# Kernel tuning notes

Measured on AMD Instinct MI355X. Metric: run time of the kernel, lower is better.

## Reference

```python
import jax, jax.numpy as jnp
import numpy as np

EMBED = 1024
D_FF = 4 * EMBED
N_EXPERTS = 8
TOP_K = 2
B, S = 2, 1024


def setup_inputs() -> dict:
    key = jax.random.key(0)
    ks = jax.random.split(key, 10)
    sc_d = 1.0 / np.sqrt(EMBED)
    sc_h = 1.0 / np.sqrt(D_FF)
    return {
        "inputs": jax.random.normal(ks[0], (B, S, EMBED), jnp.float32),
        # router MLP: Linear(D,4D) -> ReLU -> Linear(4D,E)
        "rw1": jax.random.normal(ks[1], (EMBED, D_FF), jnp.float32) * sc_d,
        "rb1": jnp.zeros((D_FF,), jnp.float32),
        "rw2": jax.random.normal(ks[2], (D_FF, N_EXPERTS), jnp.float32) * sc_h,
        "rb2": jnp.zeros((N_EXPERTS,), jnp.float32),
        # stacked expert weights: Linear(D,4D) -> ReLU -> Linear(4D,D)
        "W1": jax.random.normal(ks[3], (N_EXPERTS, EMBED, D_FF), jnp.float32) * sc_d,
        "b1": jnp.zeros((N_EXPERTS, D_FF), jnp.float32),
        "W2": jax.random.normal(ks[4], (N_EXPERTS, D_FF, EMBED), jnp.float32) * sc_h,
        "b2": jnp.zeros((N_EXPERTS, EMBED), jnp.float32),
    }


def reference(inputs, rw1, rb1, rw2, rb2, W1, b1, W2, b2):
    Bb, Ss, D = inputs.shape
    T = Bb * Ss
    xf = inputs.reshape(T, D)  # [T, D]

    # Router: scores over experts, keep top-k, softmax over kept entries only.
    score = jax.nn.relu(xf @ rw1 + rb1) @ rw2 + rb2          # [T, E]
    _, topi = jax.lax.top_k(score, TOP_K)                    # [T, K]
    mask = jnp.zeros(score.shape, bool).at[jnp.arange(T)[:, None], topi].set(True)
    gate = jax.nn.softmax(jnp.where(mask, score, -jnp.inf), axis=-1)  # [T, E]

    # Dense per-expert MLP weighted by gate; gate==0 for non-top-k experts,
    # matching the original masked gather/scatter exactly.
    out = jnp.zeros_like(xf)
    for e in range(N_EXPERTS):
        h = jax.nn.relu(xf @ W1[e] + b1[e])                  # [T, 4D]
        y = h @ W2[e] + b2[e]                                # [T, D]
        out = out + gate[:, e:e + 1] * y
    return out.reshape(Bb, Ss, D)
```

## Files before the change

### kernel.cpp

```cpp
#include <hip/hip_runtime.h>
#include <stdint.h>

typedef unsigned short ushort_t;
typedef __attribute__((ext_vector_type(8))) short short8;
typedef __attribute__((ext_vector_type(4))) float f32x4;

#define EMBED   1024
#define DFF     4096
#define NEXP    8
#define TOKENS  2048
#define SLOTS   4096
#define TMAX    40
#define TG      ((TMAX + 7) / 8)

__device__ __forceinline__ ushort_t f2bf(float f) {
  unsigned u = __float_as_uint(f);
  u += 0x7FFFu + ((u >> 16) & 1u);
  return (ushort_t)(u >> 16);
}
__device__ __forceinline__ float bf2f(ushort_t b) {
  return __uint_as_float(((unsigned)b) << 16);
}

__device__ __forceinline__ void gl2lds16(const void* g, void* l) {
  typedef const __attribute__((address_space(1))) unsigned char* gp_t;
  typedef __attribute__((address_space(3))) unsigned char* lp_t;
  __builtin_amdgcn_global_load_lds((gp_t)(uintptr_t)g, (lp_t)(uintptr_t)l, 16, 0, 0);
}

__device__ __forceinline__ void transp_body(const float* __restrict__ src,
                                            ushort_t* __restrict__ dst,
                                            int src_ld, int dst_ld, int bx, int by,
                                            int dst_koff, int lo, float (*t)[65])
{
  int n0 = bx * 64, k0 = by * 64;
  int tid = threadIdx.x;
  int kk = tid >> 4, nn = (tid & 15) * 4;
  #pragma unroll
  for (int it = 0; it < 4; it++) {
    float4 v = *(const float4*)(src + (size_t)(k0 + kk + it * 16) * src_ld + n0 + nn);
    t[kk + it * 16][nn]     = v.x;
    t[kk + it * 16][nn + 1] = v.y;
    t[kk + it * 16][nn + 2] = v.z;
    t[kk + it * 16][nn + 3] = v.w;
  }
  __syncthreads();
  int nn2 = tid >> 3, kk2 = (tid & 7) * 8;
  #pragma unroll
  for (int it = 0; it < 2; it++) {
    int n = nn2 + it * 32;
    union { ushort_t u[8]; uint4 v; } pk;
    #pragma unroll
    for (int j = 0; j < 8; j++) {
      float xv = t[kk2 + j][n];
      ushort_t hv = f2bf(xv);
      pk.u[j] = lo ? f2bf(xv - bf2f(hv)) : hv;
    }
    *(uint4*)(dst + (size_t)(n0 + n) * dst_ld + dst_koff + k0 + kk2) = pk.v;
  }
}

__global__ void transp_conv(const float* __restrict__ src, ushort_t* __restrict__ dst,
                            int src_ld, int dst_ld, long src_estride, long dst_estride,
                            int dst_koff, int lo)
{
  __shared__ __align__(16) float t[64][65];
  transp_body(src + (size_t)blockIdx.z * src_estride,
              dst + (size_t)blockIdx.z * dst_estride,
              src_ld, dst_ld, blockIdx.x, blockIdx.y, dst_koff, lo, t);
}

__global__ __launch_bounds__(256) void prep_kernel(const float* __restrict__ x,
    ushort_t* __restrict__ Xs, const float* __restrict__ rw1,
    ushort_t* __restrict__ RW1t, int* __restrict__ counts)
{
  __shared__ __align__(16) float tt[64][65];
  int bid = blockIdx.x;
  if (bid < TOKENS) {
    if (bid == 0 && threadIdx.x < NEXP) counts[threadIdx.x] = 0;
    int d = threadIdx.x * 4;
    float4 v = *(const float4*)(x + (size_t)bid * EMBED + d);
    ushort4 hi, lo;
    hi.x = f2bf(v.x); lo.x = f2bf(v.x - bf2f(hi.x));
    hi.y = f2bf(v.y); lo.y = f2bf(v.y - bf2f(hi.y));
    hi.z = f2bf(v.z); lo.z = f2bf(v.z - bf2f(hi.z));
    hi.w = f2bf(v.w); lo.w = f2bf(v.w - bf2f(hi.w));
    ushort_t* row = Xs + (size_t)bid * 2048;
    *(ushort4*)(row + d)        = hi;
    *(ushort4*)(row + 1024 + d) = lo;
    return;
  }
  int idx = bid - TOKENS;
  int which = idx >> 10, sub = idx & 1023;
  transp_body(rw1, RW1t, DFF, 3072, sub & 63, sub >> 6, which * 1024, which == 2, tt);
}

template<int APATH, int OUTMODE, bool RELU, bool EXPERT, int SPLITK, int NX, int NFUSE>
__global__ __launch_bounds__(256, 3)
void gemm_kernel(const ushort_t* __restrict__ A, const ushort_t* __restrict__ B,
                 const float* __restrict__ bias, void* __restrict__ Cout,
                 const float* __restrict__ slot_gate, const int* __restrict__ slot_token,
                 const int* __restrict__ off, const int* __restrict__ tile_e,
                 const int* __restrict__ tile_y, int e0, int e1,
                 int M, int N, int K, int ngb,
                 const float* __restrict__ tsrc0, ushort_t* __restrict__ tdst0,
                 const float* __restrict__ tsrc1, ushort_t* __restrict__ tdst1)
{
  __shared__ __align__(16) char lds_raw[49152];
  auto As = (ushort_t(*)[4096])lds_raw;
  auto Bs = (ushort_t(*)[4096])(lds_raw + 24576);

  if constexpr (NFUSE > 0) {
    int bidf = blockIdx.x;
    if (bidf >= ngb) {
      int idx = bidf - ngb;
      auto tt = (float(*)[65])lds_raw;
      const size_t ES = (size_t)EMBED * DFF;
      if (idx < 64 * 16 * 8) {
        int bx = idx & 63, by = (idx >> 6) & 15, z = idx >> 10;
        transp_body(tsrc0 + z * ES, tdst0 + z * ES, DFF, EMBED, bx, by, 0, 0, tt);
      } else {
        idx -= 64 * 16 * 8;
        int bx = idx & 15, by = (idx >> 4) & 63, z = idx >> 10;
        transp_body(tsrc1 + z * ES, tdst1 + z * ES, EMBED, DFF, bx, by, 0, 0, tt);
      }
      return;
    }
  }

  int e = 0, kc = 0, row0, col0, m_base, m_cnt;
  if (EXPERT) {
    constexpr int INNER = NX * SPLITK;
    int bid = blockIdx.x;
    int xcd = bid & 7;
    int j   = bid >> 3;
    int t   = xcd + 8 * (j / INNER);
    int i   = j % INNER;
    int xi  = i % NX;
    kc      = i / NX;
    e = tile_e[t];
    if (e < e0 || e >= e1) return;
    row0   = tile_y[t] * 128;
    col0   = xi * 128;
    m_base = off[e];
    m_cnt  = off[e + 1] - m_base;
  } else {
    int bid = blockIdx.x;
    row0 = (bid >> 5) * 128;
    col0 = (bid & 31) * 128;
    m_base = 0; m_cnt = M;
    if (row0 >= m_cnt) return;
  }
  const int Kc   = K / SPLITK;
  const int kbeg = kc * Kc;

  const int tid  = threadIdx.x;
  const int lane = tid & 63;
  const int wid  = tid >> 6;
  const int wm = wid & 1, wn = wid >> 1;

  const int srow  = lane >> 2;
  const int schk8 = ((lane & 3) ^ ((lane >> 3) & 3)) * 8;

  const ushort_t* gA[2];
  const ushort_t* gB[2];
  int aoff[2];
  const ushort_t* Bt = B + (EXPERT ? (size_t)(e - e0) * (size_t)N * K : 0);
  #pragma unroll
  for (int h = 0; h < 2; h++) {
    int r  = row0 + h * 64 + wid * 16 + srow;
    int rl = min(r, m_cnt - 1);
    size_t rowb;
    if (APATH == 2)      rowb = (size_t)slot_token[m_base + rl] * 2048;
    else if (APATH == 1) rowb = (size_t)rl * 2048;
    else                 rowb = (size_t)(m_base + rl) * (size_t)K;
    gA[h]   = A + rowb + (APATH == 0 ? kbeg : 0) + schk8;
    aoff[h] = (h * 64 + wid * 16) * 32;

    int n = col0 + h * 64 + wid * 16 + srow;
    gB[h] = Bt + (size_t)n * K + kbeg + schk8;
  }

  auto stage = [&](int pb, int kt) {
    const int k0 = kt << 5;
    const int k0a = (APATH == 1 && k0 >= 2048) ? k0 - 2048 : k0;
    #pragma unroll
    for (int h = 0; h < 2; h++) {
      gl2lds16(gA[h] + k0a, &As[pb][aoff[h]]);
      gl2lds16(gB[h] + k0,  &Bs[pb][aoff[h]]);
    }
  };

  f32x4 acc[4][4];
  #pragma unroll
  for (int i = 0; i < 4; i++)
    #pragma unroll
    for (int j = 0; j < 4; j++)
      acc[i][j] = (f32x4){0.f, 0.f, 0.f, 0.f};

  const int q  = lane >> 4;
  const int rr = lane & 15;
  const int sw8 = (q ^ ((rr >> 1) & 3)) * 8;
  const int abase = (wm * 64 + rr) * 32 + sw8;
  const int bbase = (wn * 64 + rr) * 32 + sw8;

  const int nkt = Kc >> 5;

  stage(0, 0);
  if (nkt > 1) stage(1, 1);

  for (int kt = 0; kt < nkt; kt++) {
    if (kt + 1 < nkt) asm volatile("s_waitcnt vmcnt(4)" ::: "memory");
    else              asm volatile("s_waitcnt vmcnt(0)" ::: "memory");
    __builtin_amdgcn_s_barrier();
    __builtin_amdgcn_sched_barrier(0);
    if (kt + 2 < nkt) stage((kt + 2) % 3, kt + 2);

    const int cur = kt % 3;
    short8 af[4], bfr[4];
    #pragma unroll
    for (int i = 0; i < 4; i++) {
      af[i]  = *(const short8*)(&As[cur][abase + i * 512]);
      bfr[i] = *(const short8*)(&Bs[cur][bbase + i * 512]);
    }
    asm volatile("s_waitcnt lgkmcnt(0)" ::: "memory");
    __builtin_amdgcn_sched_barrier(0);
    #pragma unroll
    for (int mt = 0; mt < 4; mt++)
      #pragma unroll
      for (int nt = 0; nt < 4; nt++)
        acc[mt][nt] = __builtin_amdgcn_mfma_f32_16x16x32_bf16(af[mt], bfr[nt], acc[mt][nt], 0, 0, 0);
  }

  const float* biasp = bias + (EXPERT ? (size_t)e * N : 0);
  float bv[4];
  #pragma unroll
  for (int nt = 0; nt < 4; nt++)
    bv[nt] = biasp[col0 + wn * 64 + nt * 16 + rr];
  const float bscale = (SPLITK == 1 || kc == 0) ? 1.f : 0.f;

  if constexpr (OUTMODE == 4) {
    const float* rw2p = slot_gate;
    float4 wa[4], wb[4];
    #pragma unroll
    for (int nt = 0; nt < 4; nt++) {
      int c = col0 + wn * 64 + nt * 16 + rr;
      wa[nt] = *(const float4*)(rw2p + (size_t)c * 8);
      wb[nt] = *(const float4*)(rw2p + (size_t)c * 8 + 4);
    }
    float* Ps = (float*)Cout;
    const int xi2 = (col0 >> 6) + wn;
    #pragma unroll
    for (int mt = 0; mt < 4; mt++) {
      #pragma unroll
      for (int i = 0; i < 4; i++) {
        float4 sA = {0.f, 0.f, 0.f, 0.f}, sB = {0.f, 0.f, 0.f, 0.f};
        #pragma unroll
        for (int nt = 0; nt < 4; nt++) {
          float v = acc[mt][nt][i] + bv[nt];
          if (RELU) v = fmaxf(v, 0.f);
          sA.x += v * wa[nt].x; sA.y += v * wa[nt].y;
          sA.z += v * wa[nt].z; sA.w += v * wa[nt].w;
          sB.x += v * wb[nt].x; sB.y += v * wb[nt].y;
          sB.z += v * wb[nt].z; sB.w += v * wb[nt].w;
        }
        #pragma unroll
        for (int o = 1; o <= 8; o <<= 1) {
          sA.x += __shfl_xor(sA.x, o); sA.y += __shfl_xor(sA.y, o);
          sA.z += __shfl_xor(sA.z, o); sA.w += __shfl_xor(sA.w, o);
          sB.x += __shfl_xor(sB.x, o); sB.y += __shfl_xor(sB.y, o);
          sB.z += __shfl_xor(sB.z, o); sB.w += __shfl_xor(sB.w, o);
        }
        if (rr == 0) {
          int row = row0 + wm * 64 + mt * 16 + q * 4 + i;
          float* p = Ps + ((size_t)row * 64 + xi2) * 8;
          *(float4*)p       = sA;
          *(float4*)(p + 4) = sB;
        }
      }
    }
  } else {
    #pragma unroll
    for (int mt = 0; mt < 4; mt++) {
      #pragma unroll
      for (int i = 0; i < 4; i++) {
        int r_loc = row0 + wm * 64 + mt * 16 + q * 4 + i;
        if (r_loc < m_cnt) {
          int slot = m_base + r_loc;
          float g = 1.f;
          if (OUTMODE == 3) g = slot_gate[slot];
          #pragma unroll
          for (int nt = 0; nt < 4; nt++) {
            float v = acc[mt][nt][i] + bscale * bv[nt];
            if (RELU) v = fmaxf(v, 0.f);
            int c = col0 + wn * 64 + nt * 16 + rr;
            if (OUTMODE == 0)      ((float*)Cout)[(size_t)slot * N + c]    = v;
            else if (OUTMODE == 1) ((ushort_t*)Cout)[(size_t)slot * N + c] = f2bf(v);
            else ((float*)Cout)[((size_t)kc * SLOTS + slot) * N + c] = g * v;
          }
        }
      }
    }
  }
}

__global__ void router_reduce(const float* __restrict__ Ps, const float* __restrict__ rb2,
                              int* __restrict__ topi, float* __restrict__ gates,
                              int* __restrict__ counts)
{
  int t = blockIdx.x * 4 + (threadIdx.x >> 6);
  if (t >= TOKENS) return;
  int lane = threadIdx.x & 63;
  const float* pt = Ps + (size_t)t * 512;
  float4 v0 = *(const float4*)(pt + lane * 8);
  float4 v1 = *(const float4*)(pt + lane * 8 + 4);
  #pragma unroll
  for (int o = 1; o <= 32; o <<= 1) {
    v0.x += __shfl_xor(v0.x, o); v0.y += __shfl_xor(v0.y, o);
    v0.z += __shfl_xor(v0.z, o); v0.w += __shfl_xor(v0.w, o);
    v1.x += __shfl_xor(v1.x, o); v1.y += __shfl_xor(v1.y, o);
    v1.z += __shfl_xor(v1.z, o); v1.w += __shfl_xor(v1.w, o);
  }
  if (lane == 0) {
    float s[8] = {v0.x + rb2[0], v0.y + rb2[1], v0.z + rb2[2], v0.w + rb2[3],
                  v1.x + rb2[4], v1.y + rb2[5], v1.z + rb2[6], v1.w + rb2[7]};
    int i0 = 0;
    #pragma unroll
    for (int e = 1; e < 8; e++) if (s[e] > s[i0]) i0 = e;
    int i1 = (i0 == 0) ? 1 : 0;
    #pragma unroll
    for (int e = 0; e < 8; e++) if (e != i0 && s[e] > s[i1]) i1 = e;
    float ex = __expf(s[i1] - s[i0]);
    float g0 = 1.f / (1.f + ex);
    float g1 = ex / (1.f + ex);
    topi[t * 2] = i0; topi[t * 2 + 1] = i1;
    gates[t * 2] = g0; gates[t * 2 + 1] = g1;
    atomicAdd(&counts[i0], 1);
    atomicAdd(&counts[i1], 1);
  }
}

__global__ void assign_all(const int* __restrict__ counts, const int* __restrict__ topi,
                           const float* __restrict__ gates, int* __restrict__ off,
                           int* __restrict__ tile_e, int* __restrict__ tile_y,
                           int* __restrict__ slot_token, float* __restrict__ slot_gate,
                           int* __restrict__ tok_slot)
{
  __shared__ int s_off[NEXP];
  __shared__ int s_cur[NEXP];
  int tid = threadIdx.x;
  if (tid < NEXP) s_cur[tid] = 0;
  if (tid == 0) {
    int a = 0, t = 0;
    for (int e = 0; e < NEXP; e++) {
      off[e] = a; s_off[e] = a;
      int c = counts[e]; a += c;
      int ty = (c + 127) >> 7;
      for (int y = 0; y < ty; y++) { tile_e[t] = e; tile_y[t] = y; t++; }
    }
    off[NEXP] = a;
    for (; t < TMAX; t++) { tile_e[t] = -1; tile_y[t] = 0; }
  }
  __syncthreads();
  for (int t = tid; t < TOKENS; t += 256) {
    #pragma unroll
    for (int k = 0; k < 2; k++) {
      int e = topi[t * 2 + k];
      int p = atomicAdd(&s_cur[e], 1);
      int s = s_off[e] + p;
      slot_token[s] = t;
      slot_gate[s]  = gates[t * 2 + k];
      tok_slot[t * 2 + k] = s;
    }
  }
}

template<int NC>
__global__ void combine_out(const float* __restrict__ Ys, const int* __restrict__ tok_slot,
                            float* __restrict__ out)
{
  int t = blockIdx.x;
  int d = threadIdx.x * 4;
  int s0 = tok_slot[t * 2], s1 = tok_slot[t * 2 + 1];
  float4 o = {0.f, 0.f, 0.f, 0.f};
  #pragma unroll
  for (int k = 0; k < NC; k++) {
    float4 a = *(const float4*)(Ys + ((size_t)k * SLOTS + s0) * EMBED + d);
    float4 b = *(const float4*)(Ys + ((size_t)k * SLOTS + s1) * EMBED + d);
    o.x += a.x + b.x;
    o.y += a.y + b.y;
    o.z += a.z + b.z;
    o.w += a.w + b.w;
  }
  *(float4*)(out + (size_t)t * EMBED + d) = o;
}

extern "C" void kernel_launch(void* const* d_in, const int* in_sizes, int n_in,
                              void* d_out, int out_size, void* d_ws, size_t ws_size,
                              hipStream_t stream)
{
  const float* x   = (const float*)d_in[0];
  const float* rw1 = (const float*)d_in[1];
  const float* rb1 = (const float*)d_in[2];
  const float* rw2 = (const float*)d_in[3];
  const float* rb2 = (const float*)d_in[4];
  const float* W1  = (const float*)d_in[5];
  const float* b1  = (const float*)d_in[6];
  const float* W2  = (const float*)d_in[7];
  const float* b2  = (const float*)d_in[8];
  float* out = (float*)d_out;
  char* ws = (char*)d_ws;

  const long W1ES = (long)EMBED * DFF;
  const long W2ES = (long)DFF * EMBED;
  const size_t SZ_R = (size_t)4096 * 4096 * 2;

  const bool FULL = ws_size >= ((size_t)300 << 20);

  if (FULL) {
    char* p = ws;
    ushort_t* W1T  = (ushort_t*)p;  p += (size_t)NEXP * DFF * EMBED * 2;
    ushort_t* W2T  = (ushort_t*)p;  p += (size_t)NEXP * EMBED * DFF * 2;
    ushort_t* RW1t = (ushort_t*)p;  p += (size_t)4096 * 3072 * 2;
    ushort_t* Hs   = (ushort_t*)p;  p += (size_t)SLOTS * DFF * 2;
    ushort_t* Xhl  = (ushort_t*)p;  p += (size_t)TOKENS * 2048 * 2;
    float*    Ys   = (float*)p;     p += (size_t)4 * SLOTS * EMBED * 4;
    float*    Ps   = (float*)p;     p += (size_t)TOKENS * 512 * 4;
    int*   topi       = (int*)p;    p += TOKENS * 2 * 4;
    float* gates      = (float*)p;  p += TOKENS * 2 * 4;
    int*   tok_slot   = (int*)p;    p += TOKENS * 2 * 4;
    int*   slot_token = (int*)p;    p += SLOTS * 4;
    float* slot_gate  = (float*)p;  p += SLOTS * 4;
    int*   counts     = (int*)p;    p += 256;
    int*   off        = (int*)p;    p += 256;
    int*   tile_e     = (int*)p;    p += 256;
    int*   tile_y     = (int*)p;    p += 256;

    prep_kernel<<<TOKENS + 3 * 1024, 256, 0, stream>>>(x, Xhl, rw1, RW1t, counts);

    gemm_kernel<1, 4, true, false, 1, 32, 2>
        <<<dim3(512 + 16384, 1, 1), 256, 0, stream>>>(Xhl, RW1t, rb1, Ps, rw2,
            nullptr, nullptr, nullptr, nullptr, 0, NEXP, TOKENS, DFF, 3072,
            512, W1, W1T, W2, W2T);

    router_reduce<<<512, 256, 0, stream>>>(Ps, rb2, topi, gates, counts);
    assign_all<<<1, 256, 0, stream>>>(counts, topi, gates, off, tile_e, tile_y,
                                      slot_token, slot_gate, tok_slot);

    gemm_kernel<2, 1, true, true, 1, 32, 0>
        <<<dim3(8 * TG * 32, 1, 1), 256, 0, stream>>>(Xhl, W1T, b1, Hs,
            nullptr, slot_token, off, tile_e, tile_y, 0, NEXP, 0, DFF, EMBED,
            0, nullptr, nullptr, nullptr, nullptr);

    gemm_kernel<0, 3, false, true, 4, 8, 0>
        <<<dim3(8 * TG * 32, 1, 1), 256, 0, stream>>>(Hs, W2T, b2, Ys,
            slot_gate, nullptr, off, tile_e, tile_y, 0, NEXP, 0, EMBED, DFF,
            0, nullptr, nullptr, nullptr, nullptr);

    combine_out<4><<<TOKENS, 256, 0, stream>>>(Ys, tok_slot, out);
  } else {
    ushort_t* RW1t = (ushort_t*)ws;
    ushort_t* WT   = (ushort_t*)ws;
    ushort_t* Hs   = (ushort_t*)(ws + SZ_R);
    ushort_t* Xhl  = (ushort_t*)(ws + 2 * SZ_R);
    float*    Ys   = (float*)(ws + 2 * SZ_R);
    char* p = ws + 3 * SZ_R;
    float* Ps         = (float*)p;  p += (size_t)TOKENS * 512 * 4;
    int*   topi       = (int*)p;    p += TOKENS * 2 * 4;
    float* gates      = (float*)p;  p += TOKENS * 2 * 4;
    int*   tok_slot   = (int*)p;    p += TOKENS * 2 * 4;
    int*   slot_token = (int*)p;    p += SLOTS * 4;
    float* slot_gate  = (float*)p;  p += SLOTS * 4;
    int*   counts     = (int*)p;    p += 256;
    int*   off        = (int*)p;    p += 256;
    int*   tile_e     = (int*)p;    p += 256;
    int*   tile_y     = (int*)p;    p += 256;

    prep_kernel<<<TOKENS + 3 * 1024, 256, 0, stream>>>(x, Xhl, rw1, RW1t, counts);

    gemm_kernel<1, 4, true, false, 1, 32, 0>
        <<<dim3(512, 1, 1), 256, 0, stream>>>(Xhl, RW1t, rb1, Ps, rw2, nullptr,
            nullptr, nullptr, nullptr, 0, NEXP, TOKENS, DFF, 3072,
            0, nullptr, nullptr, nullptr, nullptr);
    router_reduce<<<512, 256, 0, stream>>>(Ps, rb2, topi, gates, counts);
    assign_all<<<1, 256, 0, stream>>>(counts, topi, gates, off, tile_e, tile_y,
                                      slot_token, slot_gate, tok_slot);

    for (int half = 0; half < 2; half++) {
      int e0 = half * 4;
      transp_conv<<<dim3(64, 16, 4), 256, 0, stream>>>(W1 + (size_t)e0 * W1ES, WT,
          DFF, EMBED, W1ES, W1ES, 0, 0);
      gemm_kernel<2, 1, true, true, 1, 32, 0>
          <<<dim3(8 * TG * 32, 1, 1), 256, 0, stream>>>(Xhl, WT, b1, Hs,
              nullptr, slot_token, off, tile_e, tile_y, e0, e0 + 4, 0, DFF, EMBED,
              0, nullptr, nullptr, nullptr, nullptr);
    }
    for (int half = 0; half < 2; half++) {
      int e0 = half * 4;
      transp_conv<<<dim3(16, 64, 4), 256, 0, stream>>>(W2 + (size_t)e0 * W2ES, WT,
          EMBED, DFF, W2ES, W2ES, 0, 0);
      gemm_kernel<0, 3, false, true, 2, 8, 0>
          <<<dim3(8 * TG * 16, 1, 1), 256, 0, stream>>>(Hs, WT, b2, Ys,
              slot_gate, nullptr, off, tile_e, tile_y, e0, e0 + 4, 0, EMBED, DFF,
              0, nullptr, nullptr, nullptr, nullptr);
    }

    combine_out<2><<<TOKENS, 256, 0, stream>>>(Ys, tok_slot, out);
  }
}
```

Baseline: 564.1 us.

## Shrink router GEMM tile to 64 rows and move W2 transpose into expert GEMM

```diff
diff --git a/kernel.cpp b/kernel.cpp
--- a/kernel.cpp
+++ b/kernel.cpp
@@ -95,34 +95,36 @@
   transp_body(rw1, RW1t, DFF, 3072, sub & 63, sub >> 6, which * 1024, which == 2, tt);
 }
 
-template<int APATH, int OUTMODE, bool RELU, bool EXPERT, int SPLITK, int NX, int NFUSE>
-__global__ __launch_bounds__(256, 3)
+template<int MT, int APATH, int OUTMODE, bool RELU, bool EXPERT, int SPLITK, int NX, int TSHAPE>
+__global__ __launch_bounds__(256, (MT == 64 ? 4 : 3))
 void gemm_kernel(const ushort_t* __restrict__ A, const ushort_t* __restrict__ B,
                  const float* __restrict__ bias, void* __restrict__ Cout,
                  const float* __restrict__ slot_gate, const int* __restrict__ slot_token,
                  const int* __restrict__ off, const int* __restrict__ tile_e,
                  const int* __restrict__ tile_y, int e0, int e1,
                  int M, int N, int K, int ngb,
-                 const float* __restrict__ tsrc0, ushort_t* __restrict__ tdst0,
-                 const float* __restrict__ tsrc1, ushort_t* __restrict__ tdst1)
-{
-  __shared__ __align__(16) char lds_raw[49152];
-  auto As = (ushort_t(*)[4096])lds_raw;
-  auto Bs = (ushort_t(*)[4096])(lds_raw + 24576);
-
-  if constexpr (NFUSE > 0) {
+                 const float* __restrict__ tsrc, ushort_t* __restrict__ tdst)
+{
+  constexpr int MH   = MT / 64;
+  constexpr int MACC = MT / 32;
+  constexpr int ASZ  = MT * 32;
+  constexpr int BSZ  = 128 * 32;
+  __shared__ __align__(16) char lds_raw[3 * (ASZ + BSZ) * 2];
+  auto As = (ushort_t(*)[ASZ])lds_raw;
+  auto Bs = (ushort_t(*)[BSZ])(lds_raw + 3 * ASZ * 2);
+
+  if constexpr (TSHAPE > 0) {
     int bidf = blockIdx.x;
     if (bidf >= ngb) {
       int idx = bidf - ngb;
       auto tt = (float(*)[65])lds_raw;
       const size_t ES = (size_t)EMBED * DFF;
-      if (idx < 64 * 16 * 8) {
+      if constexpr (TSHAPE == 1) {
         int bx = idx & 63, by = (idx >> 6) & 15, z = idx >> 10;
-        transp_body(tsrc0 + z * ES, tdst0 + z * ES, DFF, EMBED, bx, by, 0, 0, tt);
+        transp_body(tsrc + z * ES, tdst + z * ES, DFF, EMBED, bx, by, 0, 0, tt);
       } else {
-        idx -= 64 * 16 * 8;
         int bx = idx & 15, by = (idx >> 4) & 63, z = idx >> 10;
-        transp_body(tsrc1 + z * ES, tdst1 + z * ES, EMBED, DFF, bx, by, 0, 0, tt);
+        transp_body(tsrc + z * ES, tdst + z * ES, EMBED, DFF, bx, by, 0, 0, tt);
       }
       return;
     }
@@ -146,7 +148,7 @@
     m_cnt  = off[e + 1] - m_base;
   } else {
     int bid = blockIdx.x;
-    row0 = (bid >> 5) * 128;
+    row0 = (bid >> 5) * MT;
     col0 = (bid & 31) * 128;
     m_base = 0; m_cnt = M;
     if (row0 >= m_cnt) return;
@@ -164,10 +166,10 @@
 
   const ushort_t* gA[2];
   const ushort_t* gB[2];
-  int aoff[2];
+  int aoff[2], boff[2];
   const ushort_t* Bt = B + (EXPERT ? (size_t)(e - e0) * (size_t)N * K : 0);
   #pragma unroll
-  for (int h = 0; h < 2; h++) {
+  for (int h = 0; h < MH; h++) {
     int r  = row0 + h * 64 + wid * 16 + srow;
     int rl = min(r, m_cnt - 1);
     size_t rowb;
@@ -176,24 +178,26 @@
     else                 rowb = (size_t)(m_base + rl) * (size_t)K;
     gA[h]   = A + rowb + (APATH == 0 ? kbeg : 0) + schk8;
     aoff[h] = (h * 64 + wid * 16) * 32;
-
+  }
+  #pragma unroll
+  for (int h = 0; h < 2; h++) {
     int n = col0 + h * 64 + wid * 16 + srow;
-    gB[h] = Bt + (size_t)n * K + kbeg + schk8;
+    gB[h]   = Bt + (size_t)n * K + kbeg + schk8;
+    boff[h] = (h * 64 + wid * 16) * 32;
   }
 
   auto stage = [&](int pb, int kt) {
     const int k0 = kt << 5;
     const int k0a = (APATH == 1 && k0 >= 2048) ? k0 - 2048 : k0;
     #pragma unroll
-    for (int h = 0; h < 2; h++) {
-      gl2lds16(gA[h] + k0a, &As[pb][aoff[h]]);
-      gl2lds16(gB[h] + k0,  &Bs[pb][aoff[h]]);
-    }
+    for (int h = 0; h < MH; h++) gl2lds16(gA[h] + k0a, &As[pb][aoff[h]]);
+    #pragma unroll
+    for (int h = 0; h < 2; h++)  gl2lds16(gB[h] + k0,  &Bs[pb][boff[h]]);
   };
 
-  f32x4 acc[4][4];
-  #pragma unroll
-  for (int i = 0; i < 4; i++)
+  f32x4 acc[MACC][4];
+  #pragma unroll
+  for (int i = 0; i < MACC; i++)
     #pragma unroll
     for (int j = 0; j < 4; j++)
       acc[i][j] = (f32x4){0.f, 0.f, 0.f, 0.f};
@@ -201,7 +205,7 @@
   const int q  = lane >> 4;
   const int rr = lane & 15;
   const int sw8 = (q ^ ((rr >> 1) & 3)) * 8;
-  const int abase = (wm * 64 + rr) * 32 + sw8;
+  const int abase = (wm * (MT / 2) + rr) * 32 + sw8;
   const int bbase = (wn * 64 + rr) * 32 + sw8;
 
   const int nkt = Kc >> 5;
@@ -210,23 +214,28 @@
   if (nkt > 1) stage(1, 1);
 
   for (int kt = 0; kt < nkt; kt++) {
-    if (kt + 1 < nkt) asm volatile("s_waitcnt vmcnt(4)" ::: "memory");
-    else              asm volatile("s_waitcnt vmcnt(0)" ::: "memory");
+    if (kt + 1 < nkt) {
+      if constexpr (MT == 128) asm volatile("s_waitcnt vmcnt(4)" ::: "memory");
+      else                     asm volatile("s_waitcnt vmcnt(3)" ::: "memory");
+    } else {
+      asm volatile("s_waitcnt vmcnt(0)" ::: "memory");
+    }
     __builtin_amdgcn_s_barrier();
     __builtin_amdgcn_sched_barrier(0);
     if (kt + 2 < nkt) stage((kt + 2) % 3, kt + 2);
 
     const int cur = kt % 3;
-    short8 af[4], bfr[4];
-    #pragma unroll
-    for (int i = 0; i < 4; i++) {
+    short8 af[MACC], bfr[4];
+    #pragma unroll
+    for (int i = 0; i < MACC; i++)
       af[i]  = *(const short8*)(&As[cur][abase + i * 512]);
+    #pragma unroll
+    for (int i = 0; i < 4; i++)
       bfr[i] = *(const short8*)(&Bs[cur][bbase + i * 512]);
-    }
     asm volatile("s_waitcnt lgkmcnt(0)" ::: "memory");
     __builtin_amdgcn_sched_barrier(0);
     #pragma unroll
-    for (int mt = 0; mt < 4; mt++)
+    for (int mt = 0; mt < MACC; mt++)
       #pragma unroll
       for (int nt = 0; nt < 4; nt++)
         acc[mt][nt] = __builtin_amdgcn_mfma_f32_16x16x32_bf16(af[mt], bfr[nt], acc[mt][nt], 0, 0, 0);
@@ -251,7 +260,7 @@
     float* Ps = (float*)Cout;
     const int xi2 = (col0 >> 6) + wn;
     #pragma unroll
-    for (int mt = 0; mt < 4; mt++) {
+    for (int mt = 0; mt < MACC; mt++) {
       #pragma unroll
       for (int i = 0; i < 4; i++) {
         float4 sA = {0.f, 0.f, 0.f, 0.f}, sB = {0.f, 0.f, 0.f, 0.f};
@@ -272,7 +281,7 @@
           sB.z += __shfl_xor(sB.z, o); sB.w += __shfl_xor(sB.w, o);
         }
         if (rr == 0) {
-          int row = row0 + wm * 64 + mt * 16 + q * 4 + i;
+          int row = row0 + wm * (MT / 2) + mt * 16 + q * 4 + i;
           float* p = Ps + ((size_t)row * 64 + xi2) * 8;
           *(float4*)p       = sA;
           *(float4*)(p + 4) = sB;
@@ -281,10 +290,10 @@
     }
   } else {
     #pragma unroll
-    for (int mt = 0; mt < 4; mt++) {
+    for (int mt = 0; mt < MACC; mt++) {
       #pragma unroll
       for (int i = 0; i < 4; i++) {
-        int r_loc = row0 + wm * 64 + mt * 16 + q * 4 + i;
+        int r_loc = row0 + wm * (MT / 2) + mt * 16 + q * 4 + i;
         if (r_loc < m_cnt) {
           int slot = m_base + r_loc;
           float g = 1.f;
@@ -438,24 +447,24 @@
 
     prep_kernel<<<TOKENS + 3 * 1024, 256, 0, stream>>>(x, Xhl, rw1, RW1t, counts);
 
-    gemm_kernel<1, 4, true, false, 1, 32, 2>
-        <<<dim3(512 + 16384, 1, 1), 256, 0, stream>>>(Xhl, RW1t, rb1, Ps, rw2,
+    gemm_kernel<64, 1, 4, true, false, 1, 32, 1>
+        <<<dim3(1024 + 8192, 1, 1), 256, 0, stream>>>(Xhl, RW1t, rb1, Ps, rw2,
             nullptr, nullptr, nullptr, nullptr, 0, NEXP, TOKENS, DFF, 3072,
-            512, W1, W1T, W2, W2T);
+            1024, W1, W1T);
 
     router_reduce<<<512, 256, 0, stream>>>(Ps, rb2, topi, gates, counts);
     assign_all<<<1, 256, 0, stream>>>(counts, topi, gates, off, tile_e, tile_y,
                                       slot_token, slot_gate, tok_slot);
 
-    gemm_kernel<2, 1, true, true, 1, 32, 0>
-        <<<dim3(8 * TG * 32, 1, 1), 256, 0, stream>>>(Xhl, W1T, b1, Hs,
+    gemm_kernel<128, 2, 1, true, true, 1, 32, 2>
+        <<<dim3(8 * TG * 32 + 8192, 1, 1), 256, 0, stream>>>(Xhl, W1T, b1, Hs,
             nullptr, slot_token, off, tile_e, tile_y, 0, NEXP, 0, DFF, EMBED,
-            0, nullptr, nullptr, nullptr, nullptr);
-
-    gemm_kernel<0, 3, false, true, 4, 8, 0>
+            8 * TG * 32, W2, W2T);
+
+    gemm_kernel<128, 0, 3, false, true, 4, 8, 0>
         <<<dim3(8 * TG * 32, 1, 1), 256, 0, stream>>>(Hs, W2T, b2, Ys,
             slot_gate, nullptr, off, tile_e, tile_y, 0, NEXP, 0, EMBED, DFF,
-            0, nullptr, nullptr, nullptr, nullptr);
+            0, nullptr, nullptr);
 
     combine_out<4><<<TOKENS, 256, 0, stream>>>(Ys, tok_slot, out);
   } else {
@@ -478,10 +487,10 @@
 
     prep_kernel<<<TOKENS + 3 * 1024, 256, 0, stream>>>(x, Xhl, rw1, RW1t, counts);
 
-    gemm_kernel<1, 4, true, false, 1, 32, 0>
-        <<<dim3(512, 1, 1), 256, 0, stream>>>(Xhl, RW1t, rb1, Ps, rw2, nullptr,
+    gemm_kernel<64, 1, 4, true, false, 1, 32, 0>
+        <<<dim3(1024, 1, 1), 256, 0, stream>>>(Xhl, RW1t, rb1, Ps, rw2, nullptr,
             nullptr, nullptr, nullptr, 0, NEXP, TOKENS, DFF, 3072,
-            0, nullptr, nullptr, nullptr, nullptr);
+            0, nullptr, nullptr);
     router_reduce<<<512, 256, 0, stream>>>(Ps, rb2, topi, gates, counts);
     assign_all<<<1, 256, 0, stream>>>(counts, topi, gates, off, tile_e, tile_y,
                                       slot_token, slot_gate, tok_slot);
@@ -490,19 +499,19 @@
       int e0 = half * 4;
       transp_conv<<<dim3(64, 16, 4), 256, 0, stream>>>(W1 + (size_t)e0 * W1ES, WT,
           DFF, EMBED, W1ES, W1ES, 0, 0);
-      gemm_kernel<2, 1, true, true, 1, 32, 0>
+      gemm_kernel<128, 2, 1, true, true, 1, 32, 0>
           <<<dim3(8 * TG * 32, 1, 1), 256, 0, stream>>>(Xhl, WT, b1, Hs,
               nullptr, slot_token, off, tile_e, tile_y, e0, e0 + 4, 0, DFF, EMBED,
-              0, nullptr, nullptr, nullptr, nullptr);
+              0, nullptr, nullptr);
     }
     for (int half = 0; half < 2; half++) {
       int e0 = half * 4;
       transp_conv<<<dim3(16, 64, 4), 256, 0, stream>>>(W2 + (size_t)e0 * W2ES, WT,
           EMBED, DFF, W2ES, W2ES, 0, 0);
-      gemm_kernel<0, 3, false, true, 2, 8, 0>
+      gemm_kernel<128, 0, 3, false, true, 2, 8, 0>
           <<<dim3(8 * TG * 16, 1, 1), 256, 0, stream>>>(Hs, WT, b2, Ys,
               slot_gate, nullptr, off, tile_e, tile_y, e0, e0 + 4, 0, EMBED, DFF,
-              0, nullptr, nullptr, nullptr, nullptr);
+              0, nullptr, nullptr);
     }
 
     combine_out<2><<<TOKENS, 256, 0, stream>>>(Ys, tok_slot, out);
```

Result: slower. 583.1 us (+3.4%).

## Redistribute weight transposes across GEMM launches and shrink router transpose work

Applied to the files above, without the earlier changes.

```diff
diff --git a/kernel.cpp b/kernel.cpp
--- a/kernel.cpp
+++ b/kernel.cpp
@@ -91,11 +91,38 @@
     return;
   }
   int idx = bid - TOKENS;
-  int which = idx >> 10, sub = idx & 1023;
-  transp_body(rw1, RW1t, DFF, 3072, sub & 63, sub >> 6, which * 1024, which == 2, tt);
-}
-
-template<int APATH, int OUTMODE, bool RELU, bool EXPERT, int SPLITK, int NX, int NFUSE>
+  int n0 = (idx & 63) * 64, k0 = (idx >> 6) * 64;
+  int tid = threadIdx.x;
+  int kk = tid >> 4, nn = (tid & 15) * 4;
+  #pragma unroll
+  for (int it = 0; it < 4; it++) {
+    float4 v = *(const float4*)(rw1 + (size_t)(k0 + kk + it * 16) * DFF + n0 + nn);
+    tt[kk + it * 16][nn]     = v.x;
+    tt[kk + it * 16][nn + 1] = v.y;
+    tt[kk + it * 16][nn + 2] = v.z;
+    tt[kk + it * 16][nn + 3] = v.w;
+  }
+  __syncthreads();
+  int nn2 = tid >> 3, kk2 = (tid & 7) * 8;
+  #pragma unroll
+  for (int it = 0; it < 2; it++) {
+    int n = nn2 + it * 32;
+    union { ushort_t u[8]; uint4 v; } ph, pl;
+    #pragma unroll
+    for (int j = 0; j < 8; j++) {
+      float xv = tt[kk2 + j][n];
+      ushort_t hv = f2bf(xv);
+      ph.u[j] = hv;
+      pl.u[j] = f2bf(xv - bf2f(hv));
+    }
+    ushort_t* row = RW1t + (size_t)(n0 + n) * 3072 + k0 + kk2;
+    *(uint4*)(row)        = ph.v;
+    *(uint4*)(row + 1024) = ph.v;
+    *(uint4*)(row + 2048) = pl.v;
+  }
+}
+
+template<int APATH, int OUTMODE, bool RELU, bool EXPERT, int SPLITK, int NX, int TSHAPE>
 __global__ __launch_bounds__(256, 3)
 void gemm_kernel(const ushort_t* __restrict__ A, const ushort_t* __restrict__ B,
                  const float* __restrict__ bias, void* __restrict__ Cout,
@@ -103,26 +130,24 @@
                  const int* __restrict__ off, const int* __restrict__ tile_e,
                  const int* __restrict__ tile_y, int e0, int e1,
                  int M, int N, int K, int ngb,
-                 const float* __restrict__ tsrc0, ushort_t* __restrict__ tdst0,
-                 const float* __restrict__ tsrc1, ushort_t* __restrict__ tdst1)
+                 const float* __restrict__ tsrc, ushort_t* __restrict__ tdst)
 {
   __shared__ __align__(16) char lds_raw[49152];
   auto As = (ushort_t(*)[4096])lds_raw;
   auto Bs = (ushort_t(*)[4096])(lds_raw + 24576);
 
-  if constexpr (NFUSE > 0) {
+  if constexpr (TSHAPE > 0) {
     int bidf = blockIdx.x;
     if (bidf >= ngb) {
       int idx = bidf - ngb;
       auto tt = (float(*)[65])lds_raw;
       const size_t ES = (size_t)EMBED * DFF;
-      if (idx < 64 * 16 * 8) {
+      if constexpr (TSHAPE == 1) {
         int bx = idx & 63, by = (idx >> 6) & 15, z = idx >> 10;
-        transp_body(tsrc0 + z * ES, tdst0 + z * ES, DFF, EMBED, bx, by, 0, 0, tt);
+        transp_body(tsrc + z * ES, tdst + z * ES, DFF, EMBED, bx, by, 0, 0, tt);
       } else {
-        idx -= 64 * 16 * 8;
         int bx = idx & 15, by = (idx >> 4) & 63, z = idx >> 10;
-        transp_body(tsrc1 + z * ES, tdst1 + z * ES, EMBED, DFF, bx, by, 0, 0, tt);
+        transp_body(tsrc + z * ES, tdst + z * ES, EMBED, DFF, bx, by, 0, 0, tt);
       }
       return;
     }
@@ -424,7 +449,7 @@
     ushort_t* RW1t = (ushort_t*)p;  p += (size_t)4096 * 3072 * 2;
     ushort_t* Hs   = (ushort_t*)p;  p += (size_t)SLOTS * DFF * 2;
     ushort_t* Xhl  = (ushort_t*)p;  p += (size_t)TOKENS * 2048 * 2;
-    float*    Ys   = (float*)p;     p += (size_t)4 * SLOTS * EMBED * 4;
+    float*    Ys   = (float*)p;     p += (size_t)2 * SLOTS * EMBED * 4;
     float*    Ps   = (float*)p;     p += (size_t)TOKENS * 512 * 4;
     int*   topi       = (int*)p;    p += TOKENS * 2 * 4;
     float* gates      = (float*)p;  p += TOKENS * 2 * 4;
@@ -436,28 +461,28 @@
     int*   tile_e     = (int*)p;    p += 256;
     int*   tile_y     = (int*)p;    p += 256;
 
-    prep_kernel<<<TOKENS + 3 * 1024, 256, 0, stream>>>(x, Xhl, rw1, RW1t, counts);
-
-    gemm_kernel<1, 4, true, false, 1, 32, 2>
-        <<<dim3(512 + 16384, 1, 1), 256, 0, stream>>>(Xhl, RW1t, rb1, Ps, rw2,
+    prep_kernel<<<TOKENS + 1024, 256, 0, stream>>>(x, Xhl, rw1, RW1t, counts);
+
+    gemm_kernel<1, 4, true, false, 1, 32, 1>
+        <<<dim3(512 + 8192, 1, 1), 256, 0, stream>>>(Xhl, RW1t, rb1, Ps, rw2,
             nullptr, nullptr, nullptr, nullptr, 0, NEXP, TOKENS, DFF, 3072,
-            512, W1, W1T, W2, W2T);
+            512, W1, W1T);
 
     router_reduce<<<512, 256, 0, stream>>>(Ps, rb2, topi, gates, counts);
     assign_all<<<1, 256, 0, stream>>>(counts, topi, gates, off, tile_e, tile_y,
                                       slot_token, slot_gate, tok_slot);
 
-    gemm_kernel<2, 1, true, true, 1, 32, 0>
-        <<<dim3(8 * TG * 32, 1, 1), 256, 0, stream>>>(Xhl, W1T, b1, Hs,
+    gemm_kernel<2, 1, true, true, 1, 32, 2>
+        <<<dim3(8 * TG * 32 + 8192, 1, 1), 256, 0, stream>>>(Xhl, W1T, b1, Hs,
             nullptr, slot_token, off, tile_e, tile_y, 0, NEXP, 0, DFF, EMBED,
-            0, nullptr, nullptr, nullptr, nullptr);
-
-    gemm_kernel<0, 3, false, true, 4, 8, 0>
-        <<<dim3(8 * TG * 32, 1, 1), 256, 0, stream>>>(Hs, W2T, b2, Ys,
+            8 * TG * 32, W2, W2T);
+
+    gemm_kernel<0, 3, false, true, 2, 8, 0>
+        <<<dim3(8 * TG * 16, 1, 1), 256, 0, stream>>>(Hs, W2T, b2, Ys,
             slot_gate, nullptr, off, tile_e, tile_y, 0, NEXP, 0, EMBED, DFF,
-            0, nullptr, nullptr, nullptr, nullptr);
-
-    combine_out<4><<<TOKENS, 256, 0, stream>>>(Ys, tok_slot, out);
+            0, nullptr, nullptr);
+
+    combine_out<2><<<TOKENS, 256, 0, stream>>>(Ys, tok_slot, out);
   } else {
     ushort_t* RW1t = (ushort_t*)ws;
     ushort_t* WT   = (ushort_t*)ws;
@@ -476,12 +501,12 @@
     int*   tile_e     = (int*)p;    p += 256;
     int*   tile_y     = (int*)p;    p += 256;
 
-    prep_kernel<<<TOKENS + 3 * 1024, 256, 0, stream>>>(x, Xhl, rw1, RW1t, counts);
+    prep_kernel<<<TOKENS + 1024, 256, 0, stream>>>(x, Xhl, rw1, RW1t, counts);
 
     gemm_kernel<1, 4, true, false, 1, 32, 0>
         <<<dim3(512, 1, 1), 256, 0, stream>>>(Xhl, RW1t, rb1, Ps, rw2, nullptr,
             nullptr, nullptr, nullptr, 0, NEXP, TOKENS, DFF, 3072,
-            0, nullptr, nullptr, nullptr, nullptr);
+            0, nullptr, nullptr);
     router_reduce<<<512, 256, 0, stream>>>(Ps, rb2, topi, gates, counts);
     assign_all<<<1, 256, 0, stream>>>(counts, topi, gates, off, tile_e, tile_y,
                                       slot_token, slot_gate, tok_slot);
@@ -493,7 +518,7 @@
       gemm_kernel<2, 1, true, true, 1, 32, 0>
           <<<dim3(8 * TG * 32, 1, 1), 256, 0, stream>>>(Xhl, WT, b1, Hs,
               nullptr, slot_token, off, tile_e, tile_y, e0, e0 + 4, 0, DFF, EMBED,
-              0, nullptr, nullptr, nullptr, nullptr);
+              0, nullptr, nullptr);
     }
     for (int half = 0; half < 2; half++) {
       int e0 = half * 4;
@@ -502,7 +527,7 @@
       gemm_kernel<0, 3, false, true, 2, 8, 0>
           <<<dim3(8 * TG * 16, 1, 1), 256, 0, stream>>>(Hs, WT, b2, Ys,
               slot_gate, nullptr, off, tile_e, tile_y, e0, e0 + 4, 0, EMBED, DFF,
-              0, nullptr, nullptr, nullptr, nullptr);
+              0, nullptr, nullptr);
     }
 
     combine_out<2><<<TOKENS, 256, 0, stream>>>(Ys, tok_slot, out);
```

Result: no change. 553.9 us (-1.8%).
